# Performance work log

Hardware: AMD Instinct MI355X
Metric: run time of the kernel (lower is better)

## Reference

```python
import math
import jax, jax.numpy as jnp
import numpy as np

HIDDEN = 128
NUM_REL = 48
NUM_BASES = 8
NUM_ENT = 50000
NUM_SPECIAL = 64
NUM_EDGES = 600000


def setup_inputs() -> dict:
    key = jax.random.key(0)
    ks = jax.random.split(key, 8)
    edge_index = jax.random.randint(ks[0], (2, NUM_EDGES), 0, NUM_ENT, dtype=jnp.int64)
    edge_type = jax.random.randint(ks[1], (NUM_EDGES,), 0, NUM_REL, dtype=jnp.int64)
    # node embeddings: uniform(-stdv, stdv), stdv = sqrt(6/(N+d)) as in the torch init
    stdv = math.sqrt(6.0 / (NUM_ENT + HIDDEN))
    node_embeds = jax.random.uniform(ks[2], (NUM_ENT, HIDDEN), jnp.float32, -stdv, stdv)
    # RGCN basis-decomposition params (PyG RGCNConv): weight [B, d, d], comp [R, B]
    basis = jax.random.normal(ks[3], (NUM_BASES, HIDDEN, HIDDEN), jnp.float32) * (1.0 / math.sqrt(HIDDEN))
    comp = jax.random.normal(ks[4], (NUM_REL, NUM_BASES), jnp.float32) * (1.0 / math.sqrt(NUM_BASES))
    root = jax.random.normal(ks[5], (HIDDEN, HIDDEN), jnp.float32) * (1.0 / math.sqrt(HIDDEN))
    bias = jnp.zeros((HIDDEN,), jnp.float32)
    special_emb = jax.random.normal(ks[6], (NUM_SPECIAL, HIDDEN), jnp.float32) * 0.02
    special_emb = special_emb.at[0].set(0.0)  # padding_idx=0
    return {"edge_index": edge_index, "edge_type": edge_type,
            "node_embeds": node_embeds, "basis": basis, "comp": comp,
            "root": root, "bias": bias, "special_emb": special_emb}


def rgcn_conv(x, edge_index, edge_type, basis, comp, root, bias):
    # PyG RGCNConv with basis decomposition, aggr='mean', root weight + bias.
    # W_r = sum_b comp[r, b] * basis[b]; out[n] = x[n] @ root + bias
    #        + sum_r mean_{e: type(e)=r, dst(e)=n} (x[src(e)] @ W_r)
    N = x.shape[0]
    R, B = comp.shape
    src, dst = edge_index[0], edge_index[1]
    # per-(relation, dst) in-degree for the per-relation mean aggregation
    seg = edge_type * N + dst  # [E]
    cnt = jax.ops.segment_sum(jnp.ones(src.shape[0], x.dtype), seg, num_segments=R * N)
    norm = 1.0 / jnp.maximum(cnt[seg], 1.0)  # [E]
    w = comp[edge_type] * norm[:, None]  # [E, B] per-edge basis coefficients / count
    x_src = x[src]  # [E, d] gather (dominant memory traffic)
    out = x @ root + bias  # [N, d]
    # linearity: mean over edges of (x_src @ W) == (weighted-sum of x_src) @ basis_b per basis
    for b in range(B):
        agg = jax.ops.segment_sum(x_src * w[:, b:b + 1], dst, num_segments=N)  # [N, d]
        out = out + agg @ basis[b]
    return out


def reference(edge_index, edge_type, node_embeds, basis, comp, root, bias, special_emb):
    node_out = rgcn_conv(node_embeds, edge_index, edge_type, basis, comp, root, bias)
    return jnp.concatenate([node_out, special_emb], axis=0)  # [N + S, d]
```

## Files before the change

kernel.cpp:

```cpp
#include <hip/hip_runtime.h>

#define NDIM 128
#define NBASES 8
#define KDIM 1152
#define GTILE 16
#define APITCH 1160

typedef __attribute__((ext_vector_type(8))) __bf16 bfrag;
typedef __attribute__((ext_vector_type(4))) float f32x4;

__device__ __forceinline__ float bf2f(unsigned short b) {
    return __uint_as_float(((unsigned)b) << 16);
}
__device__ __forceinline__ unsigned short f2bf(float f) {
    unsigned u = __float_as_uint(f);
    unsigned r = u + 0x7FFFu + ((u >> 16) & 1u);
    return (unsigned short)(r >> 16);
}
__device__ __forceinline__ unsigned pack2bf(float lo, float hi) {
    return (unsigned)f2bf(lo) | ((unsigned)f2bf(hi) << 16);
}
__device__ __forceinline__ float loadF(const void* p, int idx, int isf32) {
    return isf32 ? ((const float*)p)[idx] : bf2f(((const unsigned short*)p)[idx]);
}

__global__ void detect_k(const unsigned short* __restrict__ xs,
                         const int* __restrict__ ei, int* __restrict__ meta) {
    if (threadIdx.x != 0 || blockIdx.x != 0) return;
    const uint4* xv = (const uint4*)xs;
    unsigned f32m = 0;
    uint4 bx[16];
    #pragma unroll
    for (int i = 0; i < 16; ++i) bx[i] = xv[i];
    #pragma unroll
    for (int i = 0; i < 16; ++i) {
        unsigned a = bx[i].x, b = bx[i].y, c = bx[i].z, d = bx[i].w;
        f32m |= (((a & 0xFFFFu) >> 7) & 0xFFu) > 124u;
        f32m |= (((b & 0xFFFFu) >> 7) & 0xFFu) > 124u;
        f32m |= (((c & 0xFFFFu) >> 7) & 0xFFu) > 124u;
        f32m |= (((d & 0xFFFFu) >> 7) & 0xFFu) > 124u;
    }
    const uint4* ev = (const uint4*)ei;
    unsigned nzm = 0;
    for (int r = 0; r < 4; ++r) {
        uint4 be[16];
        #pragma unroll
        for (int i = 0; i < 16; ++i) be[i] = ev[r * 16 + i];
        #pragma unroll
        for (int i = 0; i < 16; ++i) nzm |= be[i].y | be[i].w;
    }
    meta[0] = f32m ? 1 : 0;
    meta[1] = nzm ? 0 : 1;
}

__global__ void misc_k(const void* __restrict__ basis, const void* __restrict__ root,
                       const void* __restrict__ se, const int* __restrict__ meta,
                       unsigned short* __restrict__ BT, void* __restrict__ out,
                       int scount, int sbase) {
    int t = blockIdx.x * 256 + threadIdx.x;
    int isf32 = meta[0];
    if (t < NDIM * KDIM) {
        int j = t / KDIM, k = t % KDIM;
        float v = (k < NBASES * NDIM) ? loadF(basis, k * NDIM + j, isf32)
                                      : loadF(root, (k - NBASES * NDIM) * NDIM + j, isf32);
        BT[t] = f2bf(v);
    } else {
        int u = t - NDIM * KDIM;
        if (u < scount) {
            float v = loadF(se, u, isf32);
            if (isf32) ((float*)out)[sbase + u] = v;
            else       ((unsigned short*)out)[sbase + u] = f2bf(v);
        }
    }
}

__global__ void hist_k(const int* __restrict__ ei, int E, int N,
                       const int* __restrict__ meta, int* __restrict__ hist) {
    int e = blockIdx.x * 256 + threadIdx.x;
    if (e >= E) return;
    int dst = meta[1] ? ei[2 * (E + e)] : ei[E + e];
    dst = min(max(dst, 0), N - 1);
    atomicAdd(&hist[dst], 1);
}

__global__ void scanA_k(const int* __restrict__ hist, int N,
                        int* __restrict__ offsets, int* __restrict__ bsum) {
    __shared__ int s[1024];
    int tid = threadIdx.x;
    int idx = blockIdx.x * 1024 + tid;
    int v = (idx < N) ? hist[idx] : 0;
    s[tid] = v;
    __syncthreads();
    for (int off = 1; off < 1024; off <<= 1) {
        int t = 0;
        if (tid >= off) t = s[tid - off];
        __syncthreads();
        if (tid >= off) s[tid] += t;
        __syncthreads();
    }
    if (idx < N) offsets[idx] = s[tid] - v;
    if (tid == 1023) bsum[blockIdx.x] = s[1023];
}
__global__ void scanB_k(const int* __restrict__ bsum, int NB, int N,
                        int* __restrict__ bpre, int* __restrict__ offsets) {
    __shared__ int s[64];
    int tid = threadIdx.x;
    int v = (tid < NB) ? bsum[tid] : 0;
    s[tid] = v;
    __syncthreads();
    for (int off = 1; off < 64; off <<= 1) {
        int t = 0;
        if (tid >= off) t = s[tid - off];
        __syncthreads();
        if (tid >= off) s[tid] += t;
        __syncthreads();
    }
    if (tid < NB) bpre[tid] = s[tid] - v;
    if (tid == NB - 1) offsets[N] = s[tid];
}
__global__ void scanC_k(int N, const int* __restrict__ bpre, int* __restrict__ offsets) {
    int idx = blockIdx.x * 1024 + threadIdx.x;
    if (idx < N) offsets[idx] += bpre[blockIdx.x];
}

__global__ void scatter_k(const int* __restrict__ ei, const int* __restrict__ et,
                          int E, int N, const int* __restrict__ meta,
                          const int* __restrict__ offsets, int* __restrict__ cursor,
                          int* __restrict__ sorted) {
    int e = blockIdx.x * 256 + threadIdx.x;
    if (e >= E) return;
    int i64 = meta[1];
    int src = i64 ? ei[2 * e] : ei[e];
    int dst = i64 ? ei[2 * (E + e)] : ei[E + e];
    int rel = i64 ? et[2 * e] : et[e];
    src = min(max(src, 0), N - 1);
    dst = min(max(dst, 0), N - 1);
    rel = rel & 63;
    int pos = offsets[dst] + atomicAdd(&cursor[dst], 1);
    sorted[pos] = src | (rel << 16);
}

__global__ __launch_bounds__(1024) void rgcn_main_k(
    const void* __restrict__ x, const void* __restrict__ comp,
    const void* __restrict__ bias, const unsigned short* __restrict__ BT,
    const int* __restrict__ meta, const int* __restrict__ offsets,
    const int* __restrict__ sorted, void* __restrict__ out, int N)
{
    __shared__ alignas(16) unsigned short A_lds[GTILE * APITCH];
    __shared__ float2 comp_lds[48 * 4];
    const int tid  = threadIdx.x;
    const int lane = tid & 63;
    const int wave = tid >> 6;
    const int isf32 = meta[0];

    for (int t = tid; t < 48 * NBASES; t += 1024)
        ((float*)comp_lds)[t] = loadF(comp, t, isf32);
    __syncthreads();

    const int nodeBase = blockIdx.x * GTILE;
    const int dg = lane & 15;
    const int bs = lane >> 4;

    {
        const int n = nodeBase + wave;
        float acc0[8], acc1[8];
        #pragma unroll
        for (int i = 0; i < 8; ++i) { acc0[i] = 0.f; acc1[i] = 0.f; }

        if (n < N) {
            const int start = offsets[n], end = offsets[n + 1];

            int myCnt = 0;
            for (int c = start; c < end; c += 64) {
                int sv = (c + lane < end) ? sorted[c + lane] : -1;
                int mm = min(64, end - c);
                for (int j = 0; j < mm; ++j) {
                    int rv = __shfl(sv, j) >> 16;
                    myCnt += (rv == lane) ? 1 : 0;
                }
            }
            float myCntF = (float)myCnt;

            if (!isf32) {
                const unsigned short* xh = (const unsigned short*)x;
                for (int c = start; c < end; c += 64) {
                    int sv = (c + lane < end) ? sorted[c + lane] : -1;
                    int mm = min(64, end - c);
                    int j = 0;
                    for (; j + 4 <= mm; j += 4) {
                        unsigned q0 = (unsigned)__shfl(sv, j);
                        unsigned q1 = (unsigned)__shfl(sv, j + 1);
                        unsigned q2 = (unsigned)__shfl(sv, j + 2);
                        unsigned q3 = (unsigned)__shfl(sv, j + 3);
                        uint4 x0 = *(const uint4*)(xh + (size_t)(q0 & 0xFFFFu) * NDIM + dg * 8);
                        uint4 x1 = *(const uint4*)(xh + (size_t)(q1 & 0xFFFFu) * NDIM + dg * 8);
                        uint4 x2 = *(const uint4*)(xh + (size_t)(q2 & 0xFFFFu) * NDIM + dg * 8);
                        uint4 x3 = *(const uint4*)(xh + (size_t)(q3 & 0xFFFFu) * NDIM + dg * 8);
                        #pragma unroll
                        for (int u = 0; u < 4; ++u) {
                            unsigned qq = (u == 0) ? q0 : (u == 1) ? q1 : (u == 2) ? q2 : q3;
                            uint4  xa = (u == 0) ? x0 : (u == 1) ? x1 : (u == 2) ? x2 : x3;
                            int rel = (int)(qq >> 16);
                            float cf = __shfl(myCntF, rel);
                            float norm = 1.0f / fmaxf(cf, 1.0f);
                            float2 cw = comp_lds[rel * 4 + bs];
                            float w0 = cw.x * norm, w1 = cw.y * norm;
                            #pragma unroll
                            for (int i = 0; i < 4; ++i) {
                                float lo = __uint_as_float(xa[i] << 16);
                                float hi = __uint_as_float(xa[i] & 0xFFFF0000u);
                                acc0[2*i]   += w0 * lo;  acc0[2*i+1] += w0 * hi;
                                acc1[2*i]   += w1 * lo;  acc1[2*i+1] += w1 * hi;
                            }
                        }
                    }
                    for (; j < mm; ++j) {
                        unsigned qq = (unsigned)__shfl(sv, j);
                        int rel = (int)(qq >> 16);
                        float cf = __shfl(myCntF, rel);
                        float norm = 1.0f / fmaxf(cf, 1.0f);
                        float2 cw = comp_lds[rel * 4 + bs];
                        float w0 = cw.x * norm, w1 = cw.y * norm;
                        uint4 xa = *(const uint4*)(xh + (size_t)(qq & 0xFFFFu) * NDIM + dg * 8);
                        #pragma unroll
                        for (int i = 0; i < 4; ++i) {
                            float lo = __uint_as_float(xa[i] << 16);
                            float hi = __uint_as_float(xa[i] & 0xFFFF0000u);
                            acc0[2*i]   += w0 * lo;  acc0[2*i+1] += w0 * hi;
                            acc1[2*i]   += w1 * lo;  acc1[2*i+1] += w1 * hi;
                        }
                    }
                }
            } else {
                const float* xf = (const float*)x;
                for (int c = start; c < end; c += 64) {
                    int sv = (c + lane < end) ? sorted[c + lane] : -1;
                    int mm = min(64, end - c);
                    for (int j = 0; j < mm; ++j) {
                        unsigned qq = (unsigned)__shfl(sv, j);
                        int rel = (int)(qq >> 16); int src = (int)(qq & 0xFFFFu);
                        float cf = __shfl(myCntF, rel);
                        float norm = 1.0f / fmaxf(cf, 1.0f);
                        float2 cw = comp_lds[rel * 4 + bs];
                        float w0 = cw.x * norm, w1 = cw.y * norm;
                        #pragma unroll
                        for (int i = 0; i < 8; ++i) {
                            float xv = xf[(size_t)src * NDIM + dg * 8 + i];
                            acc0[i] += w0 * xv; acc1[i] += w1 * xv;
                        }
                    }
                }
            }
        }

        unsigned short* row = &A_lds[wave * APITCH];
        uint4 p0, p1;
        p0.x = pack2bf(acc0[0], acc0[1]); p0.y = pack2bf(acc0[2], acc0[3]);
        p0.z = pack2bf(acc0[4], acc0[5]); p0.w = pack2bf(acc0[6], acc0[7]);
        p1.x = pack2bf(acc1[0], acc1[1]); p1.y = pack2bf(acc1[2], acc1[3]);
        p1.z = pack2bf(acc1[4], acc1[5]); p1.w = pack2bf(acc1[6], acc1[7]);
        *(uint4*)(row + (bs * 2 + 0) * NDIM + dg * 8) = p0;
        *(uint4*)(row + (bs * 2 + 1) * NDIM + dg * 8) = p1;
        if (bs == 0) {
            uint4 xr = {0, 0, 0, 0};
            if (n < N) {
                if (!isf32) {
                    xr = *(const uint4*)((const unsigned short*)x + (size_t)n * NDIM + dg * 8);
                } else {
                    const float* xf = (const float*)x + (size_t)n * NDIM + dg * 8;
                    xr.x = pack2bf(xf[0], xf[1]); xr.y = pack2bf(xf[2], xf[3]);
                    xr.z = pack2bf(xf[4], xf[5]); xr.w = pack2bf(xf[6], xf[7]);
                }
            }
            *(uint4*)(row + NBASES * NDIM + dg * 8) = xr;
        }
    }
    __syncthreads();

    if (wave < 4) {
        const int m = lane & 15;
        const int q = lane >> 4;
        f32x4 C0 = {0,0,0,0}, C1 = {0,0,0,0};
        const unsigned short* arow = &A_lds[m * APITCH];
        const int jb = wave * 32;
        for (int ks = 0; ks < KDIM / 32; ++ks) {
            int k = ks * 32 + q * 8;
            bfrag a  = *(const bfrag*)(arow + k);
            bfrag b0 = *(const bfrag*)(BT + (size_t)(jb +  0 + m) * KDIM + k);
            bfrag b1 = *(const bfrag*)(BT + (size_t)(jb + 16 + m) * KDIM + k);
            C0 = __builtin_amdgcn_mfma_f32_16x16x32_bf16(a, b0, C0, 0, 0, 0);
            C1 = __builtin_amdgcn_mfma_f32_16x16x32_bf16(a, b1, C1, 0, 0, 0);
        }
        #pragma unroll
        for (int t = 0; t < 2; ++t) {
            f32x4 Ct = t ? C1 : C0;
            int j = jb + t * 16 + m;
            float bj = loadF(bias, j, isf32);
            #pragma unroll
            for (int r = 0; r < 4; ++r) {
                int n = nodeBase + q * 4 + r;
                if (n < N) {
                    float v = Ct[r] + bj;
                    if (isf32) ((float*)out)[(size_t)n * NDIM + j] = v;
                    else       ((unsigned short*)out)[(size_t)n * NDIM + j] = f2bf(v);
                }
            }
        }
    }
}

extern "C" void kernel_launch(void* const* d_in, const int* in_sizes, int n_in,
                              void* d_out, int out_size, void* d_ws, size_t ws_size,
                              hipStream_t stream) {
    const int* ei = (const int*)d_in[0];
    const int* et = (const int*)d_in[1];

    const int E = in_sizes[1];
    const int N = in_sizes[2] / NDIM;
    const int S = in_sizes[7] / NDIM;
    const int NB = (N + 1023) / 1024;

    char* ws = (char*)d_ws;
    size_t off = 0;
    int* meta    = (int*)(ws + off); off += 16;
    int* hist    = (int*)(ws + off); off += (size_t)N * 4;
    int* cursor  = (int*)(ws + off); off += (size_t)N * 4;
    int* offsets = (int*)(ws + off); off = (off + (size_t)(N + 1) * 4 + 15) & ~(size_t)15;
    int* bsum    = (int*)(ws + off); off += 64 * 4;
    int* bpre    = (int*)(ws + off); off += 64 * 4;
    unsigned short* BT = (unsigned short*)(ws + off); off += (size_t)NDIM * KDIM * 2;
    int* sorted  = (int*)(ws + off); off += (size_t)E * 4;

    hipMemsetAsync(hist, 0, (size_t)2 * N * 4, stream);

    detect_k<<<1, 64, 0, stream>>>((const unsigned short*)d_in[2], ei, meta);
    misc_k<<<(NDIM * KDIM + S * NDIM + 255) / 256, 256, 0, stream>>>(
        d_in[3], d_in[5], d_in[7], meta, BT, d_out, S * NDIM, N * NDIM);
    hist_k<<<(E + 255) / 256, 256, 0, stream>>>(ei, E, N, meta, hist);
    scanA_k<<<NB, 1024, 0, stream>>>(hist, N, offsets, bsum);
    scanB_k<<<1, 64, 0, stream>>>(bsum, NB, N, bpre, offsets);
    scanC_k<<<NB, 1024, 0, stream>>>(N, bpre, offsets);
    scatter_k<<<(E + 255) / 256, 256, 0, stream>>>(ei, et, E, N, meta, offsets, cursor, sorted);
    rgcn_main_k<<<(N + GTILE - 1) / GTILE, 1024, 0, stream>>>(d_in[2], d_in[4], d_in[6], BT,
                                                              meta, offsets, sorted, d_out, N);
}
```

Measured before the change: 340.1 us.

## Split gather across two edge halves per wave with LDS relation counts

Each wave now handles two edges at once, one per half-wave, with each lane covering 4 feature dims and all 8 bases. Previously each edge was read by 4 lane groups that each covered 2 bases, so every row was fetched four times per wave. The half-wave partial sums are combined with a cross-lane xor shuffle before packing to LDS. Per-relation counts now come from LDS atomics plus a fast reciprocal instead of a serial shuffle loop, and the next source row is prefetched in software. The cost is higher register pressure (32 accumulators), and the launch-bounds occupancy hint is raised.

```diff
diff --git a/kernel.cpp b/kernel.cpp
--- a/kernel.cpp
+++ b/kernel.cpp
@@ -140,139 +140,126 @@
     sorted[pos] = src | (rel << 16);
 }
 
-__global__ __launch_bounds__(1024) void rgcn_main_k(
+__global__ __launch_bounds__(1024, 8) void rgcn_main_k(
     const void* __restrict__ x, const void* __restrict__ comp,
     const void* __restrict__ bias, const unsigned short* __restrict__ BT,
     const int* __restrict__ meta, const int* __restrict__ offsets,
     const int* __restrict__ sorted, void* __restrict__ out, int N)
 {
     __shared__ alignas(16) unsigned short A_lds[GTILE * APITCH];
-    __shared__ float2 comp_lds[48 * 4];
+    __shared__ alignas(16) float comp_lds[48 * NBASES];
+    __shared__ int cnt_lds[GTILE * 48];
     const int tid  = threadIdx.x;
     const int lane = tid & 63;
     const int wave = tid >> 6;
     const int isf32 = meta[0];
 
     for (int t = tid; t < 48 * NBASES; t += 1024)
-        ((float*)comp_lds)[t] = loadF(comp, t, isf32);
+        comp_lds[t] = loadF(comp, t, isf32);
     __syncthreads();
 
     const int nodeBase = blockIdx.x * GTILE;
-    const int dg = lane & 15;
-    const int bs = lane >> 4;
+    const int dl = lane & 31;
+    const int eg = lane >> 5;
 
     {
         const int n = nodeBase + wave;
-        float acc0[8], acc1[8];
-        #pragma unroll
-        for (int i = 0; i < 8; ++i) { acc0[i] = 0.f; acc1[i] = 0.f; }
+        float acc[8][4];
+        #pragma unroll
+        for (int j = 0; j < 8; ++j)
+            #pragma unroll
+            for (int i = 0; i < 4; ++i) acc[j][i] = 0.f;
+
+        int* cnt_row = &cnt_lds[wave * 48];
 
         if (n < N) {
             const int start = offsets[n], end = offsets[n + 1];
 
-            int myCnt = 0;
-            for (int c = start; c < end; c += 64) {
-                int sv = (c + lane < end) ? sorted[c + lane] : -1;
-                int mm = min(64, end - c);
-                for (int j = 0; j < mm; ++j) {
-                    int rv = __shfl(sv, j) >> 16;
-                    myCnt += (rv == lane) ? 1 : 0;
-                }
+            if (lane < 48) cnt_row[lane] = 0;
+            for (int c = start + lane; c < end; c += 64)
+                atomicAdd(&cnt_row[(sorted[c] >> 16) & 63], 1);
+            if (lane < 48) {
+                float nv = __builtin_amdgcn_rcpf(fmaxf((float)cnt_row[lane], 1.0f));
+                cnt_row[lane] = __float_as_int(nv);
             }
-            float myCntF = (float)myCnt;
 
             if (!isf32) {
                 const unsigned short* xh = (const unsigned short*)x;
-                for (int c = start; c < end; c += 64) {
-                    int sv = (c + lane < end) ? sorted[c + lane] : -1;
-                    int mm = min(64, end - c);
-                    int j = 0;
-                    for (; j + 4 <= mm; j += 4) {
-                        unsigned q0 = (unsigned)__shfl(sv, j);
-                        unsigned q1 = (unsigned)__shfl(sv, j + 1);
-                        unsigned q2 = (unsigned)__shfl(sv, j + 2);
-                        unsigned q3 = (unsigned)__shfl(sv, j + 3);
-                        uint4 x0 = *(const uint4*)(xh + (size_t)(q0 & 0xFFFFu) * NDIM + dg * 8);
-                        uint4 x1 = *(const uint4*)(xh + (size_t)(q1 & 0xFFFFu) * NDIM + dg * 8);
-                        uint4 x2 = *(const uint4*)(xh + (size_t)(q2 & 0xFFFFu) * NDIM + dg * 8);
-                        uint4 x3 = *(const uint4*)(xh + (size_t)(q3 & 0xFFFFu) * NDIM + dg * 8);
+                if (start < end) {
+                    int i0 = start + eg;
+                    unsigned q0 = (i0 < end) ? (unsigned)sorted[i0] : 0u;
+                    uint2 xa0 = *(const uint2*)(xh + (size_t)(q0 & 0xFFFFu) * NDIM + dl * 4);
+                    int i1 = start + 2 + eg;
+                    unsigned q1 = (i1 < end) ? (unsigned)sorted[i1] : 0u;
+                    for (int c = start; c < end; c += 2) {
+                        uint2 xa1 = *(const uint2*)(xh + (size_t)(q1 & 0xFFFFu) * NDIM + dl * 4);
+                        int i2 = c + 4 + eg;
+                        unsigned q2 = (i2 < end) ? (unsigned)sorted[i2] : 0u;
+                        bool act = (c + eg) < end;
+                        int rel = (int)((q0 >> 16) & 63u);
+                        float norm = act ? __int_as_float(cnt_row[rel]) : 0.f;
+                        f32x4 cwA = *(const f32x4*)&comp_lds[rel * NBASES + 4 * eg];
+                        f32x4 cwB = *(const f32x4*)&comp_lds[rel * NBASES + 4 * (1 ^ eg)];
+                        float w[8];
                         #pragma unroll
-                        for (int u = 0; u < 4; ++u) {
-                            unsigned qq = (u == 0) ? q0 : (u == 1) ? q1 : (u == 2) ? q2 : q3;
-                            uint4  xa = (u == 0) ? x0 : (u == 1) ? x1 : (u == 2) ? x2 : x3;
-                            int rel = (int)(qq >> 16);
-                            float cf = __shfl(myCntF, rel);
-                            float norm = 1.0f / fmaxf(cf, 1.0f);
-                            float2 cw = comp_lds[rel * 4 + bs];
-                            float w0 = cw.x * norm, w1 = cw.y * norm;
+                        for (int j = 0; j < 4; ++j) { w[j] = cwA[j] * norm; w[4 + j] = cwB[j] * norm; }
+                        float xf[4];
+                        xf[0] = __uint_as_float(xa0.x << 16);
+                        xf[1] = __uint_as_float(xa0.x & 0xFFFF0000u);
+                        xf[2] = __uint_as_float(xa0.y << 16);
+                        xf[3] = __uint_as_float(xa0.y & 0xFFFF0000u);
+                        #pragma unroll
+                        for (int j = 0; j < 8; ++j)
                             #pragma unroll
-                            for (int i = 0; i < 4; ++i) {
-                                float lo = __uint_as_float(xa[i] << 16);
-                                float hi = __uint_as_float(xa[i] & 0xFFFF0000u);
-                                acc0[2*i]   += w0 * lo;  acc0[2*i+1] += w0 * hi;
-                                acc1[2*i]   += w1 * lo;  acc1[2*i+1] += w1 * hi;
-                            }
-                        }
-                    }
-                    for (; j < mm; ++j) {
-                        unsigned qq = (unsigned)__shfl(sv, j);
-                        int rel = (int)(qq >> 16);
-                        float cf = __shfl(myCntF, rel);
-                        float norm = 1.0f / fmaxf(cf, 1.0f);
-                        float2 cw = comp_lds[rel * 4 + bs];
-                        float w0 = cw.x * norm, w1 = cw.y * norm;
-                        uint4 xa = *(const uint4*)(xh + (size_t)(qq & 0xFFFFu) * NDIM + dg * 8);
-                        #pragma unroll
-                        for (int i = 0; i < 4; ++i) {
-                            float lo = __uint_as_float(xa[i] << 16);
-                            float hi = __uint_as_float(xa[i] & 0xFFFF0000u);
-                            acc0[2*i]   += w0 * lo;  acc0[2*i+1] += w0 * hi;
-                            acc1[2*i]   += w1 * lo;  acc1[2*i+1] += w1 * hi;
-                        }
+                            for (int i = 0; i < 4; ++i) acc[j][i] += w[j] * xf[i];
+                        q0 = q1; xa0 = xa1; q1 = q2;
                     }
                 }
             } else {
-                const float* xf = (const float*)x;
-                for (int c = start; c < end; c += 64) {
-                    int sv = (c + lane < end) ? sorted[c + lane] : -1;
-                    int mm = min(64, end - c);
-                    for (int j = 0; j < mm; ++j) {
-                        unsigned qq = (unsigned)__shfl(sv, j);
-                        int rel = (int)(qq >> 16); int src = (int)(qq & 0xFFFFu);
-                        float cf = __shfl(myCntF, rel);
-                        float norm = 1.0f / fmaxf(cf, 1.0f);
-                        float2 cw = comp_lds[rel * 4 + bs];
-                        float w0 = cw.x * norm, w1 = cw.y * norm;
+                const float* xfp = (const float*)x;
+                for (int c = start; c < end; c += 2) {
+                    bool act = (c + eg) < end;
+                    unsigned q = act ? (unsigned)sorted[c + eg] : 0u;
+                    int rel = (int)((q >> 16) & 63u);
+                    float norm = act ? __int_as_float(cnt_row[rel]) : 0.f;
+                    f32x4 cwA = *(const f32x4*)&comp_lds[rel * NBASES + 4 * eg];
+                    f32x4 cwB = *(const f32x4*)&comp_lds[rel * NBASES + 4 * (1 ^ eg)];
+                    float w[8];
+                    #pragma unroll
+                    for (int j = 0; j < 4; ++j) { w[j] = cwA[j] * norm; w[4 + j] = cwB[j] * norm; }
+                    f32x4 xv = *(const f32x4*)(xfp + (size_t)(q & 0xFFFFu) * NDIM + dl * 4);
+                    #pragma unroll
+                    for (int j = 0; j < 8; ++j)
                         #pragma unroll
-                        for (int i = 0; i < 8; ++i) {
-                            float xv = xf[(size_t)src * NDIM + dg * 8 + i];
-                            acc0[i] += w0 * xv; acc1[i] += w1 * xv;
-                        }
-                    }
+                        for (int i = 0; i < 4; ++i) acc[j][i] += w[j] * xv[i];
                 }
             }
         }
 
         unsigned short* row = &A_lds[wave * APITCH];
-        uint4 p0, p1;
-        p0.x = pack2bf(acc0[0], acc0[1]); p0.y = pack2bf(acc0[2], acc0[3]);
-        p0.z = pack2bf(acc0[4], acc0[5]); p0.w = pack2bf(acc0[6], acc0[7]);
-        p1.x = pack2bf(acc1[0], acc1[1]); p1.y = pack2bf(acc1[2], acc1[3]);
-        p1.z = pack2bf(acc1[4], acc1[5]); p1.w = pack2bf(acc1[6], acc1[7]);
-        *(uint4*)(row + (bs * 2 + 0) * NDIM + dg * 8) = p0;
-        *(uint4*)(row + (bs * 2 + 1) * NDIM + dg * 8) = p1;
-        if (bs == 0) {
-            uint4 xr = {0, 0, 0, 0};
+        #pragma unroll
+        for (int b = 0; b < 4; ++b) {
+            float f0 = acc[b][0] + __shfl_xor(acc[4 + b][0], 32);
+            float f1 = acc[b][1] + __shfl_xor(acc[4 + b][1], 32);
+            float f2 = acc[b][2] + __shfl_xor(acc[4 + b][2], 32);
+            float f3 = acc[b][3] + __shfl_xor(acc[4 + b][3], 32);
+            uint2 p;
+            p.x = pack2bf(f0, f1);
+            p.y = pack2bf(f2, f3);
+            *(uint2*)(row + (4 * eg + b) * NDIM + dl * 4) = p;
+        }
+        if (eg == 0) {
+            uint2 xr = {0, 0};
             if (n < N) {
                 if (!isf32) {
-                    xr = *(const uint4*)((const unsigned short*)x + (size_t)n * NDIM + dg * 8);
+                    xr = *(const uint2*)((const unsigned short*)x + (size_t)n * NDIM + dl * 4);
                 } else {
-                    const float* xf = (const float*)x + (size_t)n * NDIM + dg * 8;
-                    xr.x = pack2bf(xf[0], xf[1]); xr.y = pack2bf(xf[2], xf[3]);
-                    xr.z = pack2bf(xf[4], xf[5]); xr.w = pack2bf(xf[6], xf[7]);
+                    const float* xf = (const float*)x + (size_t)n * NDIM + dl * 4;
+                    xr.x = pack2bf(xf[0], xf[1]);
+                    xr.y = pack2bf(xf[2], xf[3]);
                 }
             }
-            *(uint4*)(row + NBASES * NDIM + dg * 8) = xr;
+            *(uint2*)(row + NBASES * NDIM + dl * 4) = xr;
         }
     }
     __syncthreads();
```

New measurement: 330.2 us. 1.03x faster.
